# Kernel tuning notes

Measured on AMD Instinct MI355X. Metric: run time of the kernel, lower is better.

Reference implementation:

```python
import jax, jax.numpy as jnp
import numpy as np

# OmniNet(deepqmc) reconstruction: ElectronicSchNet v1 (2 interactions, kernel_dim=8,
# embedding_dim=16, dist_feat_dim=4) + Linear(16,1,bias=False) orbital + sum over electrons.
# SchNet v1: shared w and g per interaction, spin-dependent h (same/anti), nuclear
# messages via learned nuclear embeddings Y. Subnets: w = 2-layer log-DNN 4->6->8 with SSP,
# h = Linear(16,8), g = Linear(8,16). SSP(x) = softplus(x) - log(2).

N_UP, N_DOWN = 16, 16
N_ELEC = N_UP + N_DOWN
N_ATOMS = 8
DIST_FEAT, KERNEL, EMBED = 4, 8, 16
N_INTER = 2
BATCH = 4096


def ssp(x):
    return jax.nn.softplus(x) - jnp.log(2.0).astype(x.dtype)


def setup_inputs() -> dict:
    key = jax.random.key(0)
    ks = jax.random.split(key, 16)
    s = 0.5  # init scale
    return {
        'dists_nuc': jax.random.uniform(ks[0], (BATCH, N_ELEC, N_ATOMS, DIST_FEAT), jnp.float32),
        'dists_elec': jax.random.uniform(ks[1], (BATCH, N_ELEC, N_ELEC, DIST_FEAT), jnp.float32),
        'X': jax.random.normal(ks[2], (1, EMBED), jnp.float32) * s,          # electron embedding (n_up==n_down)
        'Y': jax.random.normal(ks[3], (N_ATOMS, KERNEL), jnp.float32) * s,   # nuclear embeddings
        'w1': jax.random.normal(ks[4], (N_INTER, DIST_FEAT, 6), jnp.float32) * s,
        'wb1': jax.random.normal(ks[5], (N_INTER, 6), jnp.float32) * s,
        'w2': jax.random.normal(ks[6], (N_INTER, 6, KERNEL), jnp.float32) * s,
        'wb2': jax.random.normal(ks[7], (N_INTER, KERNEL), jnp.float32) * s,
        'hs_w': jax.random.normal(ks[8], (N_INTER, EMBED, KERNEL), jnp.float32) * s,
        'hs_b': jax.random.normal(ks[9], (N_INTER, KERNEL), jnp.float32) * s,
        'ha_w': jax.random.normal(ks[10], (N_INTER, EMBED, KERNEL), jnp.float32) * s,
        'ha_b': jax.random.normal(ks[11], (N_INTER, KERNEL), jnp.float32) * s,
        'g_w': jax.random.normal(ks[12], (N_INTER, KERNEL, EMBED), jnp.float32) * s,
        'g_b': jax.random.normal(ks[13], (N_INTER, EMBED), jnp.float32) * s,
        'orb_w': jax.random.normal(ks[14], (EMBED,), jnp.float32) * s,
    }


def reference(dists_nuc, dists_elec, X, Y, w1, wb1, w2, wb2, hs_w, hs_b, ha_w, ha_b, g_w, g_b, orb_w):
    B, n_elec = dists_elec.shape[:2]
    dt = dists_elec.dtype
    spins = jnp.concatenate([jnp.zeros(N_UP, jnp.int32), jnp.ones(N_DOWN, jnp.int32)])
    eye = jnp.eye(n_elec, dtype=bool)
    same = ((spins[:, None] == spins[None, :]) & ~eye).astype(dt)  # (i,j) same-spin, no self
    anti = (spins[:, None] != spins[None, :]).astype(dt)

    # initial embeddings: all electrons share X[0] since n_up == n_down
    x = jnp.broadcast_to(X[0], (B, n_elec, EMBED))

    for n in range(N_INTER):
        def w_net(e):  # (..., 4) -> (..., 8)
            return ssp(e @ w1[n] + wb1[n]) @ w2[n] + wb2[n]
        we = w_net(dists_elec)            # (B, i, j, K)
        wn = w_net(dists_nuc)             # (B, i, M, K)
        hs = x @ hs_w[n] + hs_b[n]        # (B, j, K) same-spin message features
        ha = x @ ha_w[n] + ha_b[n]        # (B, j, K) anti-spin
        z = (jnp.einsum('bijk,ij,bjk->bik', we, same, hs)
             + jnp.einsum('bijk,ij,bjk->bik', we, anti, ha)
             + jnp.einsum('bimk,mk->bik', wn, Y))
        x = x + (z @ g_w[n] + g_b[n])     # residual update

    # orbital projection (Linear(16,1,bias=False)), squeeze, sum over electrons
    return (x @ orb_w).sum(axis=-1)       # (B,)
```

## Files before the change

kernel.cpp:

```cpp
#include <hip/hip_runtime.h>

#define NE 32
#define NA 8
#define DF 4
#define KD 8
#define ED 16
#define BATCH 4096

#define WS_W1S0 0
#define WS_W1S1 24
#define WS_B1S0 48
#define WS_B1S1 54
#define WS_B2H0 60
#define WS_B2H1 68
#define WS_MS0  76
#define WS_MA0  84
#define WS_MS   92
#define WS_MA   156
#define WS_CS   220
#define WS_CA   228
#define WS_GO0  236
#define WS_GO1  244
#define WS_BASE 252

typedef float f32x2 __attribute__((ext_vector_type(2)));
__device__ __forceinline__ f32x2 splat2(float s) { f32x2 r; r.x = s; r.y = s; return r; }
__device__ __forceinline__ f32x2 fma2(f32x2 a, f32x2 b, f32x2 c) {
    return __builtin_elementwise_fma(a, b, c);
}

__global__ void omni_setup(const float* __restrict__ X,   const float* __restrict__ w1,
                           const float* __restrict__ wb1, const float* __restrict__ w2,
                           const float* __restrict__ wb2, const float* __restrict__ hs_w,
                           const float* __restrict__ hs_b,const float* __restrict__ ha_w,
                           const float* __restrict__ ha_b,const float* __restrict__ g_w,
                           const float* __restrict__ g_b, const float* __restrict__ orb_w,
                           float* __restrict__ ws)
{
    const int t = threadIdx.x;
    const float L   = 1.4426950408889634f;
    const float LN2 = 0.6931471805599453f;
    if (t < 48) {
        ws[t] = w1[t] * L;
    } else if (t < 60) {
        ws[t] = wb1[t - 48] * L;
    } else if (t < 76) {
        const int u = t - 60, n = u >> 3, k = u & 7;
        float sw = 0.f;
        for (int a = 0; a < 6; ++a) sw += w2[n * 48 + a * KD + k];
        ws[t] = wb2[n * KD + k] * L - sw;
    } else if (t < 92) {
        const int u = t - 76, tab = u >> 3, k = u & 7;
        const float* mw = tab ? ha_w : hs_w;
        const float* mb = tab ? ha_b : hs_b;
        float acc = mb[k];
        for (int c = 0; c < ED; ++c) acc += X[c] * mw[c * KD + k];
        ws[t] = acc;
    } else if (t < 220) {
        int u = t - 92; const int tab = u >> 6; u &= 63;
        const int kp = u >> 3, k = u & 7;
        const float* mw = (tab ? ha_w : hs_w) + ED * KD;
        float acc = 0.f;
        for (int c = 0; c < ED; ++c)
            acc += LN2 * g_w[kp * ED + c] * mw[c * KD + k];
        ws[t] = acc;
    } else if (t < 236) {
        const int u = t - 220, tab = u >> 3, k = u & 7;
        const float* mw = (tab ? ha_w : hs_w) + ED * KD;
        const float* mb = (tab ? ha_b : hs_b) + KD;
        float acc = mb[k];
        for (int c = 0; c < ED; ++c) acc += (X[c] + g_b[c]) * mw[c * KD + k];
        ws[t] = acc;
    } else if (t < 252) {
        const int u = t - 236, n = u >> 3, k = u & 7;
        float acc = 0.f;
        for (int c = 0; c < ED; ++c)
            acc += LN2 * g_w[n * KD * ED + k * ED + c] * orb_w[c];
        ws[t] = acc;
    } else if (t == 252) {
        float acc = 0.f;
        for (int c = 0; c < ED; ++c) acc += (X[c] + g_b[c] + g_b[ED + c]) * orb_w[c];
        ws[t] = acc;
    }
}

__device__ __forceinline__ void wnet_r2(const float4 e,
                                        const f32x2* __restrict__ vB1s2,
                                        const f32x2* __restrict__ sW12,
                                        f32x2* __restrict__ r2)
{
    #pragma unroll
    for (int a2 = 0; a2 < 3; ++a2) {
        f32x2 u = fma2(splat2(e.x), sW12[a2], vB1s2[a2]);
        u = fma2(splat2(e.y), sW12[3 + a2], u);
        u = fma2(splat2(e.z), sW12[6 + a2], u);
        u = fma2(splat2(e.w), sW12[9 + a2], u);
        f32x2 t;
        t.x = __builtin_amdgcn_exp2f(u.x);
        t.y = __builtin_amdgcn_exp2f(u.y);
        t = t + splat2(1.0f);
        r2[a2].x = __builtin_amdgcn_logf(t.x);
        r2[a2].y = __builtin_amdgcn_logf(t.y);
    }
}

__device__ __forceinline__ void proj2(const f32x2* __restrict__ r2,
                                      const f32x2* __restrict__ sW22,
                                      const f32x2* __restrict__ vB2h2,
                                      f32x2* __restrict__ racc2)
{
    #pragma unroll
    for (int k2 = 0; k2 < 4; ++k2) {
        f32x2 acc = vB2h2[k2];
        acc = fma2(splat2(r2[0].x), sW22[0 * 4 + k2], acc);
        acc = fma2(splat2(r2[0].y), sW22[1 * 4 + k2], acc);
        acc = fma2(splat2(r2[1].x), sW22[2 * 4 + k2], acc);
        acc = fma2(splat2(r2[1].y), sW22[3 * 4 + k2], acc);
        acc = fma2(splat2(r2[2].x), sW22[4 * 4 + k2], acc);
        acc = fma2(splat2(r2[2].y), sW22[5 * 4 + k2], acc);
        racc2[k2] = acc;
    }
}

__global__ __launch_bounds__(128)
__attribute__((amdgpu_waves_per_eu(4, 4)))
void omni_main(
    const float* __restrict__ dists_nuc,
    const float* __restrict__ dists_elec,
    const float* __restrict__ Y,
    const float* __restrict__ w2,
    const float* __restrict__ ws,
    float* __restrict__ out)
{
    const int tid  = threadIdx.x;
    const int h    = tid >> 6;
    const int lane = tid & 63;
    const int il   = lane & 15;
    const int jh   = lane >> 4;
    const int ig   = 16 * h + il;
    const int b    = blockIdx.x;
    const int sj   = jh >> 1;
    const bool same = (sj == h);
    const int t32  = same ? 0 : 32;

    __shared__ float4 ebuf[8 * 128];
    __shared__ float msg[65][KD];
    __shared__ float part[2];
    if (tid < KD) msg[64][tid] = 0.0f;

    const f32x2* ws2  = (const f32x2*)ws;
    const f32x2* w2p0 = (const f32x2*)w2;
    const f32x2* w2p1 = (const f32x2*)(w2 + 48);
    const f32x2* Yp   = (const f32x2*)Y;

    const float* de = dists_elec + (((size_t)b * NE + ig) * NE + 8 * jh) * DF;
    const float* dn = dists_nuc  + (((size_t)b * NE + ig) * NA + 2 * jh) * DF;

    const float4 nr0 = ((const float4*)dn)[0];
    const float4 nr1 = ((const float4*)dn)[1];

    float zr0[KD];
    {
        f32x2 vB1s2[3], vB2h2[4], msel2[4];
        #pragma unroll
        for (int a2 = 0; a2 < 3; ++a2) vB1s2[a2] = ws2[WS_B1S0 / 2 + a2];
        #pragma unroll
        for (int k2 = 0; k2 < 4; ++k2) vB2h2[k2] = ws2[WS_B2H0 / 2 + k2];
        #pragma unroll
        for (int k2 = 0; k2 < 4; ++k2)
            msel2[k2] = same ? ws2[WS_MS0 / 2 + k2] : ws2[WS_MA0 / 2 + k2];

        const int scnt  = ig - 8 * jh;
        const float fcnt = (jh == (ig >> 3)) ? 7.0f : 8.0f;
        f32x2 S2[3] = {splat2(0.f), splat2(0.f), splat2(0.f)};
        #pragma unroll
        for (int s = 0; s < 8; ++s) {
            const float4 e = ((const float4*)de)[s];
            ebuf[s * 128 + tid] = e;
            f32x2 r2[3];
            wnet_r2(e, vB1s2, ws2 + WS_W1S0 / 2, r2);
            const float mf = (s == scnt) ? 0.0f : 1.0f;
            #pragma unroll
            for (int a2 = 0; a2 < 3; ++a2) S2[a2] = fma2(r2[a2], splat2(mf), S2[a2]);
        }
        f32x2 z2[4];
        #pragma unroll
        for (int k2 = 0; k2 < 4; ++k2) {
            f32x2 acc = splat2(fcnt) * vB2h2[k2];
            acc = fma2(splat2(S2[0].x), w2p0[0 * 4 + k2], acc);
            acc = fma2(splat2(S2[0].y), w2p0[1 * 4 + k2], acc);
            acc = fma2(splat2(S2[1].x), w2p0[2 * 4 + k2], acc);
            acc = fma2(splat2(S2[1].y), w2p0[3 * 4 + k2], acc);
            acc = fma2(splat2(S2[2].x), w2p0[4 * 4 + k2], acc);
            acc = fma2(splat2(S2[2].y), w2p0[5 * 4 + k2], acc);
            z2[k2] = acc * msel2[k2];
        }
        {
            f32x2 r2[3], racc2[4];
            wnet_r2(nr0, vB1s2, ws2 + WS_W1S0 / 2, r2);
            proj2(r2, w2p0, vB2h2, racc2);
            #pragma unroll
            for (int k2 = 0; k2 < 4; ++k2)
                z2[k2] = fma2(racc2[k2], Yp[(2 * jh) * 4 + k2], z2[k2]);
            wnet_r2(nr1, vB1s2, ws2 + WS_W1S0 / 2, r2);
            proj2(r2, w2p0, vB2h2, racc2);
            #pragma unroll
            for (int k2 = 0; k2 < 4; ++k2)
                z2[k2] = fma2(racc2[k2], Yp[(2 * jh + 1) * 4 + k2], z2[k2]);
        }
        #pragma unroll
        for (int k2 = 0; k2 < 4; ++k2) {
            float za = z2[k2].x, zb = z2[k2].y;
            za += __shfl_xor(za, 16, 64); za += __shfl_xor(za, 32, 64);
            zb += __shfl_xor(zb, 16, 64); zb += __shfl_xor(zb, 32, 64);
            zr0[2 * k2] = za; zr0[2 * k2 + 1] = zb;
        }
    }

    {
        f32x2 ms2[4], ma2[4];
        #pragma unroll
        for (int k2 = 0; k2 < 4; ++k2) {
            ms2[k2] = ws2[WS_CS / 2 + k2];
            ma2[k2] = ws2[WS_CA / 2 + k2];
        }
        #pragma unroll
        for (int kp = 0; kp < KD; ++kp) {
            const f32x2 zk = splat2(zr0[kp]);
            #pragma unroll
            for (int k2 = 0; k2 < 4; ++k2) {
                ms2[k2] = fma2(zk, ws2[WS_MS / 2 + kp * 4 + k2], ms2[k2]);
                ma2[k2] = fma2(zk, ws2[WS_MA / 2 + kp * 4 + k2], ma2[k2]);
            }
        }
        if (jh == 0) {
            #pragma unroll
            for (int k2 = 0; k2 < 4; ++k2) *(f32x2*)&msg[ig][2 * k2] = ms2[k2];
        } else if (jh == 2) {
            #pragma unroll
            for (int k2 = 0; k2 < 4; ++k2) *(f32x2*)&msg[32 + ig][2 * k2] = ma2[k2];
        }
        __syncthreads();
    }

    float zr1[KD];
    {
        f32x2 vB1s2[3], vB2h2[4];
        #pragma unroll
        for (int a2 = 0; a2 < 3; ++a2) vB1s2[a2] = ws2[WS_B1S1 / 2 + a2];
        #pragma unroll
        for (int k2 = 0; k2 < 4; ++k2) vB2h2[k2] = ws2[WS_B2H1 / 2 + k2];

        f32x2 z2[4] = {splat2(0.f), splat2(0.f), splat2(0.f), splat2(0.f)};
        #pragma unroll
        for (int s = 0; s < 8; ++s) {
            const float4 e = ebuf[s * 128 + tid];
            f32x2 r2[3], racc2[4];
            wnet_r2(e, vB1s2, ws2 + WS_W1S1 / 2, r2);
            proj2(r2, w2p1, vB2h2, racc2);
            const int j = 8 * jh + s;
            const int row = (j == ig) ? 64 : (t32 + j);
            const f32x2* mrow = (const f32x2*)&msg[row][0];
            #pragma unroll
            for (int k2 = 0; k2 < 4; ++k2) z2[k2] = fma2(racc2[k2], mrow[k2], z2[k2]);
        }
        {
            f32x2 r2[3], racc2[4];
            wnet_r2(nr0, vB1s2, ws2 + WS_W1S1 / 2, r2);
            proj2(r2, w2p1, vB2h2, racc2);
            #pragma unroll
            for (int k2 = 0; k2 < 4; ++k2)
                z2[k2] = fma2(racc2[k2], Yp[(2 * jh) * 4 + k2], z2[k2]);
            wnet_r2(nr1, vB1s2, ws2 + WS_W1S1 / 2, r2);
            proj2(r2, w2p1, vB2h2, racc2);
            #pragma unroll
            for (int k2 = 0; k2 < 4; ++k2)
                z2[k2] = fma2(racc2[k2], Yp[(2 * jh + 1) * 4 + k2], z2[k2]);
        }
        #pragma unroll
        for (int k2 = 0; k2 < 4; ++k2) {
            float za = z2[k2].x, zb = z2[k2].y;
            za += __shfl_xor(za, 16, 64); za += __shfl_xor(za, 32, 64);
            zb += __shfl_xor(zb, 16, 64); zb += __shfl_xor(zb, 32, 64);
            zr1[2 * k2] = za; zr1[2 * k2 + 1] = zb;
        }
    }

    float dot = 0.0f;
    #pragma unroll
    for (int k = 0; k < KD; ++k) dot = fmaf(zr0[k], ws[WS_GO0 + k], dot);
    #pragma unroll
    for (int k = 0; k < KD; ++k) dot = fmaf(zr1[k], ws[WS_GO1 + k], dot);
    dot += ws[WS_BASE];
    dot *= 0.25f;
    #pragma unroll
    for (int off = 1; off < 64; off <<= 1) dot += __shfl_xor(dot, off, 64);
    if (lane == 0) part[h] = dot;
    __syncthreads();
    if (tid == 0) out[b] = part[0] + part[1];
}

extern "C" void kernel_launch(void* const* d_in, const int* in_sizes, int n_in,
                              void* d_out, int out_size, void* d_ws, size_t ws_size,
                              hipStream_t stream) {
    const float* dists_nuc  = (const float*)d_in[0];
    const float* dists_elec = (const float*)d_in[1];
    const float* X     = (const float*)d_in[2];
    const float* Y     = (const float*)d_in[3];
    const float* w1    = (const float*)d_in[4];
    const float* wb1   = (const float*)d_in[5];
    const float* w2    = (const float*)d_in[6];
    const float* wb2   = (const float*)d_in[7];
    const float* hs_w  = (const float*)d_in[8];
    const float* hs_b  = (const float*)d_in[9];
    const float* ha_w  = (const float*)d_in[10];
    const float* ha_b  = (const float*)d_in[11];
    const float* g_w   = (const float*)d_in[12];
    const float* g_b   = (const float*)d_in[13];
    const float* orb_w = (const float*)d_in[14];
    float* out = (float*)d_out;
    float* ws  = (float*)d_ws;

    omni_setup<<<1, 256, 0, stream>>>(X, w1, wb1, w2, wb2, hs_w, hs_b,
                                      ha_w, ha_b, g_w, g_b, orb_w, ws);
    omni_main<<<BATCH, 128, 0, stream>>>(dists_nuc, dists_elec, Y, w2, ws, out);
}
```

Before: 144.3 us.

## Split each electron row across eight lanes with 256-thread blocks

Doubles the block size to 256 threads so each lane handles 4 electron partners and 1 nucleus instead of 8 and 2. Each electron's row is now spread over 8 lanes, which needs one extra cross-lane shuffle step per reduction, and the fixed waves-per-EU attribute is removed. The per-thread serial work and register use should drop and more threads are exposed for latency hiding. The cost is more shuffles and the redundant per-lane weight loads and message-feature math being duplicated across twice as many threads. The first-layer dot product is also moved before the barrier.

```diff
diff --git a/kernel.cpp b/kernel.cpp
--- a/kernel.cpp
+++ b/kernel.cpp
@@ -122,9 +122,7 @@
     }
 }
 
-__global__ __launch_bounds__(128)
-__attribute__((amdgpu_waves_per_eu(4, 4)))
-void omni_main(
+__global__ __launch_bounds__(256) void omni_main(
     const float* __restrict__ dists_nuc,
     const float* __restrict__ dists_elec,
     const float* __restrict__ Y,
@@ -133,19 +131,20 @@
     float* __restrict__ out)
 {
     const int tid  = threadIdx.x;
-    const int h    = tid >> 6;
+    const int w    = tid >> 6;
     const int lane = tid & 63;
-    const int il   = lane & 15;
-    const int jh   = lane >> 4;
-    const int ig   = 16 * h + il;
+    const int ie   = lane & 7;
+    const int joct = lane >> 3;
+    const int ig   = 8 * w + ie;
     const int b    = blockIdx.x;
-    const int sj   = jh >> 1;
+    const int h    = ig >> 4;
+    const int sj   = joct >> 2;
     const bool same = (sj == h);
     const int t32  = same ? 0 : 32;
 
-    __shared__ float4 ebuf[8 * 128];
+    __shared__ float4 ebuf[4 * 256];
     __shared__ float msg[65][KD];
-    __shared__ float part[2];
+    __shared__ float part[4];
     if (tid < KD) msg[64][tid] = 0.0f;
 
     const f32x2* ws2  = (const f32x2*)ws;
@@ -153,11 +152,11 @@
     const f32x2* w2p1 = (const f32x2*)(w2 + 48);
     const f32x2* Yp   = (const f32x2*)Y;
 
-    const float* de = dists_elec + (((size_t)b * NE + ig) * NE + 8 * jh) * DF;
-    const float* dn = dists_nuc  + (((size_t)b * NE + ig) * NA + 2 * jh) * DF;
-
-    const float4 nr0 = ((const float4*)dn)[0];
-    const float4 nr1 = ((const float4*)dn)[1];
+    const float* de = dists_elec + (((size_t)b * NE + ig) * NE + 4 * joct) * DF;
+    const float* dn = dists_nuc  + (((size_t)b * NE + ig) * NA + joct) * DF;
+    const float4* de4 = (const float4*)de;
+
+    const float4 nr0 = *(const float4*)dn;
 
     float zr0[KD];
     {
@@ -170,13 +169,13 @@
         for (int k2 = 0; k2 < 4; ++k2)
             msel2[k2] = same ? ws2[WS_MS0 / 2 + k2] : ws2[WS_MA0 / 2 + k2];
 
-        const int scnt  = ig - 8 * jh;
-        const float fcnt = (jh == (ig >> 3)) ? 7.0f : 8.0f;
+        const int scnt  = ig - 4 * joct;
+        const float fcnt = (joct == (ig >> 2)) ? 3.0f : 4.0f;
         f32x2 S2[3] = {splat2(0.f), splat2(0.f), splat2(0.f)};
         #pragma unroll
-        for (int s = 0; s < 8; ++s) {
-            const float4 e = ((const float4*)de)[s];
-            ebuf[s * 128 + tid] = e;
+        for (int s = 0; s < 4; ++s) {
+            const float4 e = de4[s];
+            ebuf[s * 256 + tid] = e;
             f32x2 r2[3];
             wnet_r2(e, vB1s2, ws2 + WS_W1S0 / 2, r2);
             const float mf = (s == scnt) ? 0.0f : 1.0f;
@@ -201,18 +200,13 @@
             proj2(r2, w2p0, vB2h2, racc2);
             #pragma unroll
             for (int k2 = 0; k2 < 4; ++k2)
-                z2[k2] = fma2(racc2[k2], Yp[(2 * jh) * 4 + k2], z2[k2]);
-            wnet_r2(nr1, vB1s2, ws2 + WS_W1S0 / 2, r2);
-            proj2(r2, w2p0, vB2h2, racc2);
-            #pragma unroll
-            for (int k2 = 0; k2 < 4; ++k2)
-                z2[k2] = fma2(racc2[k2], Yp[(2 * jh + 1) * 4 + k2], z2[k2]);
+                z2[k2] = fma2(racc2[k2], Yp[joct * 4 + k2], z2[k2]);
         }
         #pragma unroll
         for (int k2 = 0; k2 < 4; ++k2) {
             float za = z2[k2].x, zb = z2[k2].y;
-            za += __shfl_xor(za, 16, 64); za += __shfl_xor(za, 32, 64);
-            zb += __shfl_xor(zb, 16, 64); zb += __shfl_xor(zb, 32, 64);
+            za += __shfl_xor(za, 8, 64); za += __shfl_xor(za, 16, 64); za += __shfl_xor(za, 32, 64);
+            zb += __shfl_xor(zb, 8, 64); zb += __shfl_xor(zb, 16, 64); zb += __shfl_xor(zb, 32, 64);
             zr0[2 * k2] = za; zr0[2 * k2 + 1] = zb;
         }
     }
@@ -233,15 +227,20 @@
                 ma2[k2] = fma2(zk, ws2[WS_MA / 2 + kp * 4 + k2], ma2[k2]);
             }
         }
-        if (jh == 0) {
+        if (joct == 0) {
             #pragma unroll
             for (int k2 = 0; k2 < 4; ++k2) *(f32x2*)&msg[ig][2 * k2] = ms2[k2];
-        } else if (jh == 2) {
+        } else if (joct == 4) {
             #pragma unroll
             for (int k2 = 0; k2 < 4; ++k2) *(f32x2*)&msg[32 + ig][2 * k2] = ma2[k2];
         }
-        __syncthreads();
-    }
+    }
+
+    float dot = ws[WS_BASE];
+    #pragma unroll
+    for (int k = 0; k < KD; ++k) dot = fmaf(zr0[k], ws[WS_GO0 + k], dot);
+
+    __syncthreads();
 
     float zr1[KD];
     {
@@ -253,12 +252,12 @@
 
         f32x2 z2[4] = {splat2(0.f), splat2(0.f), splat2(0.f), splat2(0.f)};
         #pragma unroll
-        for (int s = 0; s < 8; ++s) {
-            const float4 e = ebuf[s * 128 + tid];
+        for (int s = 0; s < 4; ++s) {
+            const float4 e = ebuf[s * 256 + tid];
             f32x2 r2[3], racc2[4];
             wnet_r2(e, vB1s2, ws2 + WS_W1S1 / 2, r2);
             proj2(r2, w2p1, vB2h2, racc2);
-            const int j = 8 * jh + s;
+            const int j = 4 * joct + s;
             const int row = (j == ig) ? 64 : (t32 + j);
             const f32x2* mrow = (const f32x2*)&msg[row][0];
             #pragma unroll
@@ -270,34 +269,25 @@
             proj2(r2, w2p1, vB2h2, racc2);
             #pragma unroll
             for (int k2 = 0; k2 < 4; ++k2)
-                z2[k2] = fma2(racc2[k2], Yp[(2 * jh) * 4 + k2], z2[k2]);
-            wnet_r2(nr1, vB1s2, ws2 + WS_W1S1 / 2, r2);
-            proj2(r2, w2p1, vB2h2, racc2);
-            #pragma unroll
-            for (int k2 = 0; k2 < 4; ++k2)
-                z2[k2] = fma2(racc2[k2], Yp[(2 * jh + 1) * 4 + k2], z2[k2]);
+                z2[k2] = fma2(racc2[k2], Yp[joct * 4 + k2], z2[k2]);
         }
         #pragma unroll
         for (int k2 = 0; k2 < 4; ++k2) {
             float za = z2[k2].x, zb = z2[k2].y;
-            za += __shfl_xor(za, 16, 64); za += __shfl_xor(za, 32, 64);
-            zb += __shfl_xor(zb, 16, 64); zb += __shfl_xor(zb, 32, 64);
+            za += __shfl_xor(za, 8, 64); za += __shfl_xor(za, 16, 64); za += __shfl_xor(za, 32, 64);
+            zb += __shfl_xor(zb, 8, 64); zb += __shfl_xor(zb, 16, 64); zb += __shfl_xor(zb, 32, 64);
             zr1[2 * k2] = za; zr1[2 * k2 + 1] = zb;
         }
     }
 
-    float dot = 0.0f;
-    #pragma unroll
-    for (int k = 0; k < KD; ++k) dot = fmaf(zr0[k], ws[WS_GO0 + k], dot);
     #pragma unroll
     for (int k = 0; k < KD; ++k) dot = fmaf(zr1[k], ws[WS_GO1 + k], dot);
-    dot += ws[WS_BASE];
-    dot *= 0.25f;
+    dot *= 0.125f;
     #pragma unroll
     for (int off = 1; off < 64; off <<= 1) dot += __shfl_xor(dot, off, 64);
-    if (lane == 0) part[h] = dot;
+    if (lane == 0) part[w] = dot;
     __syncthreads();
-    if (tid == 0) out[b] = part[0] + part[1];
+    if (tid == 0) out[b] = part[0] + part[1] + part[2] + part[3];
 }
 
 extern "C" void kernel_launch(void* const* d_in, const int* in_sizes, int n_in,
@@ -323,5 +313,5 @@
 
     omni_setup<<<1, 256, 0, stream>>>(X, w1, wb1, w2, wb2, hs_w, hs_b,
                                       ha_w, ha_b, g_w, g_b, orb_w, ws);
-    omni_main<<<BATCH, 128, 0, stream>>>(dists_nuc, dists_elec, Y, w2, ws, out);
-}
+    omni_main<<<BATCH, 256, 0, stream>>>(dists_nuc, dists_elec, Y, w2, ws, out);
+}
```

Measured after the change: 146.0 us. Within noise of the previous version (+1.2%).
